# Kernel tuning notes

Hardware: AMD Instinct MI355X
Metric: run time of the kernel (lower is better)

## Reference

```python
import jax, jax.numpy as jnp
import numpy as np
import math

GRID = 14  # coords run 1..13 -> 13x13 spatial grid
Z = math.exp(math.log(2.0 * math.pi) + 1.0)
EPS = 1e-06

def setup_inputs() -> dict:
    key = jax.random.key(0)
    B, C = 256, 1024
    x = jax.random.normal(key, (B, GRID - 1, GRID - 1, C), dtype=jnp.float32)
    return {"feature_input": x}

def reference(feature_input) -> jnp.ndarray:
    B, H, W, C = feature_input.shape
    f = jax.nn.softmax(feature_input, axis=3)  # softmax over channel dim (dim=3)
    coords = jnp.arange(1, GRID, dtype=jnp.float32)  # [13]
    xv = coords[:, None]  # varies along spatial axis 0 (torch meshgrid 'ij')
    yv = coords[None, :]  # varies along spatial axis 1
    s = f.sum(axis=(1, 2)) + EPS  # [B, C] per-slice mass
    # soft-argmax centroids, [B, C]
    mx = (xv[None, :, :, None] * f).sum(axis=(1, 2)) / s
    my = (yv[None, :, :, None] * f).sum(axis=(1, 2)) / s
    # weighted variances, normalized by 169 and the per-slice mass
    dx2 = (xv[None, :, :, None] - mx[:, None, None, :]) ** 2
    dy2 = (yv[None, :, :, None] - my[:, None, None, :]) ** 2
    x_var = (dx2 * f).sum(axis=(1, 2)) / 169.0 / s
    y_var = (dy2 * f).sum(axis=(1, 2)) / 169.0 / s
    det_xy = (x_var + y_var) ** 2 * Z  # [B, C]
    return det_xy.sum() / B / C
```

## Files before the change

kernel.cpp:

```cpp
#include <hip/hip_runtime.h>

#ifndef __has_builtin
#define __has_builtin(x) 0
#endif

__device__ __forceinline__ float fast_exp2(float x) {
#if __has_builtin(__builtin_amdgcn_exp2f)
    return __builtin_amdgcn_exp2f(x);
#else
    return exp2f(x);
#endif
}

__device__ __forceinline__ float fast_log2(float x) {
#if __has_builtin(__builtin_amdgcn_logf)
    return __builtin_amdgcn_logf(x);
#else
    return log2f(x);
#endif
}

constexpr int   kB      = 256;
constexpr int   kC      = 1024;
constexpr int   kG      = 13;
constexpr int   kP      = kG * kG;
constexpr float kEps    = 1e-6f;
constexpr float kZ      = 17.079468445347132f;
constexpr float kLog2e  = 1.4426950408889634f;
constexpr float kInv169 = 1.0f / 169.0f;
constexpr float kScale  = 1.0f / (256.0f * 1024.0f);

__global__ __launch_bounds__(1024, 4)
void constrain_loss_fused(const float* __restrict__ x, float* __restrict__ out)
{
    __shared__ float snL[kP];
    __shared__ float sred[16];

    const int tid  = threadIdx.x;
    const int lane = tid & 63;
    const int wid  = tid >> 6;
    const int b    = blockIdx.x;

    const float* __restrict__ xb = x + (size_t)b * kP * kC;

    for (int p = wid; p < kP; p += 16) {
        const float4* __restrict__ src = (const float4*)(xb + (size_t)p * kC);
        float4 v0 = src[lane];
        float4 v1 = src[lane + 64];
        float4 v2 = src[lane + 128];
        float4 v3 = src[lane + 192];

        float s =
            (fast_exp2(v0.x * kLog2e) + fast_exp2(v0.y * kLog2e)) +
            (fast_exp2(v0.z * kLog2e) + fast_exp2(v0.w * kLog2e)) +
            (fast_exp2(v1.x * kLog2e) + fast_exp2(v1.y * kLog2e)) +
            (fast_exp2(v1.z * kLog2e) + fast_exp2(v1.w * kLog2e)) +
            (fast_exp2(v2.x * kLog2e) + fast_exp2(v2.y * kLog2e)) +
            (fast_exp2(v2.z * kLog2e) + fast_exp2(v2.w * kLog2e)) +
            (fast_exp2(v3.x * kLog2e) + fast_exp2(v3.y * kLog2e)) +
            (fast_exp2(v3.z * kLog2e) + fast_exp2(v3.w * kLog2e));

        #pragma unroll
        for (int m = 1; m < 64; m <<= 1)
            s += __shfl_xor(s, m);

        if (lane == 0) snL[p] = -fast_log2(s);
    }
    __syncthreads();

    const float* __restrict__ xc = xb + tid;

    float S0 = 0.f, S1x = 0.f, S2x = 0.f, S1y = 0.f, S2y = 0.f;

    #pragma unroll
    for (int h = 0; h < kG; ++h) {
        const float* __restrict__ row = xc + (size_t)h * kG * kC;
        float v[kG];
        #pragma unroll
        for (int w = 0; w < kG; ++w)
            v[w] = row[(size_t)w * kC];

        float t0 = 0.f, t1 = 0.f, t2 = 0.f;
        #pragma unroll
        for (int w = 0; w < kG; ++w) {
            const float e = fast_exp2(fmaf(v[w], kLog2e, snL[h * kG + w]));
            t0 += e;
            t1 = fmaf((float)(w + 1), e, t1);
            t2 = fmaf((float)((w + 1) * (w + 1)), e, t2);
        }
        const float fx = (float)(h + 1);
        S0  += t0;
        S1x  = fmaf(fx,      t0, S1x);
        S2x  = fmaf(fx * fx, t0, S2x);
        S1y += t1;
        S2y += t2;
    }

    const float s   = S0 + kEps;
    const float is  = 1.0f / s;
    const float mx  = S1x * is;
    const float my  = S1y * is;
    const float nx  = S2x - mx * (2.0f * S1x - mx * S0);
    const float ny  = S2y - my * (2.0f * S1y - my * S0);
    const float t   = (nx + ny) * is * kInv169;
    float det = t * t * kZ;

    #pragma unroll
    for (int m = 1; m < 64; m <<= 1)
        det += __shfl_xor(det, m);

    if (lane == 0) sred[wid] = det;
    __syncthreads();
    if (wid == 0) {
        float v = (lane < 16) ? sred[lane] : 0.0f;
        #pragma unroll
        for (int m = 1; m < 16; m <<= 1)
            v += __shfl_xor(v, m);
        if (lane == 0) atomicAdd(out, v * kScale);
    }
}

extern "C" void kernel_launch(void* const* d_in, const int* in_sizes, int n_in,
                              void* d_out, int out_size, void* d_ws, size_t ws_size,
                              hipStream_t stream)
{
    const float* x   = (const float*)d_in[0];
    float*       out = (float*)d_out;

    hipMemsetAsync(out, 0, sizeof(float) * (size_t)out_size, stream);
    constrain_loss_fused<<<dim3(kB), dim3(1024), 0, stream>>>(x, out);
}
```

Measured before the change: 263.7 us.

## Split spatial positions across four blocks per batch with register-resident single pass

Each batch is split into four blocks over spatial positions. Each thread keeps its exp values in registers, so the input is read and exponentiated once instead of twice. Partial moments go to a workspace and a second kernel combines them into the loss. This raises block count for better occupancy, at the cost of an extra launch, workspace traffic and possible register pressure.

```diff
diff --git a/kernel.cpp b/kernel.cpp
--- a/kernel.cpp
+++ b/kernel.cpp
@@ -12,18 +12,12 @@
 #endif
 }
 
-__device__ __forceinline__ float fast_log2(float x) {
-#if __has_builtin(__builtin_amdgcn_logf)
-    return __builtin_amdgcn_logf(x);
-#else
-    return log2f(x);
-#endif
-}
-
 constexpr int   kB      = 256;
 constexpr int   kC      = 1024;
 constexpr int   kG      = 13;
 constexpr int   kP      = kG * kG;
+constexpr int   kParts  = 4;
+constexpr int   kMaxPP  = 43;
 constexpr float kEps    = 1e-6f;
 constexpr float kZ      = 17.079468445347132f;
 constexpr float kLog2e  = 1.4426950408889634f;
@@ -31,9 +25,83 @@
 constexpr float kScale  = 1.0f / (256.0f * 1024.0f);
 
 __global__ __launch_bounds__(1024, 4)
-void constrain_loss_fused(const float* __restrict__ x, float* __restrict__ out)
+void part_stats_kernel(const float* __restrict__ x, float* __restrict__ ws)
 {
-    __shared__ float snL[kP];
+    __shared__ float4 sTab[kP];
+    __shared__ float  sP[kMaxPP * 16];
+    __shared__ float  sInvD[kMaxPP];
+
+    const int tid   = threadIdx.x;
+    const int lane  = tid & 63;
+    const int wid   = tid >> 6;
+    const int b     = blockIdx.x >> 2;
+    const int part  = blockIdx.x & 3;
+    const int start = part * 42;
+    const bool full = (part == 3);
+
+    if (tid < kP) {
+        const int h = tid / kG;
+        const int w = tid - h * kG;
+        const float fx = (float)(h + 1);
+        const float fy = (float)(w + 1);
+        sTab[tid] = make_float4(fx, fy, fx * fx, fy * fy);
+    }
+
+    const float* __restrict__ xc = x + (size_t)b * kP * kC + (size_t)start * kC + tid;
+
+    float e[kMaxPP];
+    #pragma unroll
+    for (int i = 0; i < kMaxPP; ++i)
+        e[i] = xc[(size_t)i * kC];
+
+    #pragma unroll
+    for (int i = 0; i < kMaxPP; ++i)
+        e[i] = fast_exp2(e[i] * kLog2e);
+
+    if (!full) e[42] = 0.0f;
+
+    #pragma unroll
+    for (int i = 0; i < kMaxPP; ++i) {
+        float s = e[i];
+        #pragma unroll
+        for (int m = 1; m < 64; m <<= 1)
+            s += __shfl_xor(s, m);
+        if (lane == 0) sP[i * 16 + wid] = s;
+    }
+    __syncthreads();
+
+    if (tid < kMaxPP) {
+        float d = 0.f;
+        #pragma unroll
+        for (int w = 0; w < 16; ++w)
+            d += sP[tid * 16 + w];
+        sInvD[tid] = 1.0f / (d + 1e-30f);
+    }
+    __syncthreads();
+
+    float S0 = 0.f, S1x = 0.f, S1y = 0.f, S2x = 0.f, S2y = 0.f;
+    #pragma unroll
+    for (int i = 0; i < kMaxPP; ++i) {
+        const float  f = e[i] * sInvD[i];
+        const float4 t = sTab[start + i];
+        S0  += f;
+        S1x  = fmaf(t.x, f, S1x);
+        S1y  = fmaf(t.y, f, S1y);
+        S2x  = fmaf(t.z, f, S2x);
+        S2y  = fmaf(t.w, f, S2y);
+    }
+
+    float* __restrict__ o = ws + (((size_t)part * kB + b) * 5) * kC + tid;
+    o[0 * kC] = S0;
+    o[1 * kC] = S1x;
+    o[2 * kC] = S1y;
+    o[3 * kC] = S2x;
+    o[4 * kC] = S2y;
+}
+
+__global__ __launch_bounds__(1024, 4)
+void combine_kernel(const float* __restrict__ ws, float* __restrict__ out)
+{
     __shared__ float sred[16];
 
     const int tid  = threadIdx.x;
@@ -41,59 +109,15 @@
     const int wid  = tid >> 6;
     const int b    = blockIdx.x;
 
-    const float* __restrict__ xb = x + (size_t)b * kP * kC;
-
-    for (int p = wid; p < kP; p += 16) {
-        const float4* __restrict__ src = (const float4*)(xb + (size_t)p * kC);
-        float4 v0 = src[lane];
-        float4 v1 = src[lane + 64];
-        float4 v2 = src[lane + 128];
-        float4 v3 = src[lane + 192];
-
-        float s =
-            (fast_exp2(v0.x * kLog2e) + fast_exp2(v0.y * kLog2e)) +
-            (fast_exp2(v0.z * kLog2e) + fast_exp2(v0.w * kLog2e)) +
-            (fast_exp2(v1.x * kLog2e) + fast_exp2(v1.y * kLog2e)) +
-            (fast_exp2(v1.z * kLog2e) + fast_exp2(v1.w * kLog2e)) +
-            (fast_exp2(v2.x * kLog2e) + fast_exp2(v2.y * kLog2e)) +
-            (fast_exp2(v2.z * kLog2e) + fast_exp2(v2.w * kLog2e)) +
-            (fast_exp2(v3.x * kLog2e) + fast_exp2(v3.y * kLog2e)) +
-            (fast_exp2(v3.z * kLog2e) + fast_exp2(v3.w * kLog2e));
-
-        #pragma unroll
-        for (int m = 1; m < 64; m <<= 1)
-            s += __shfl_xor(s, m);
-
-        if (lane == 0) snL[p] = -fast_log2(s);
-    }
-    __syncthreads();
-
-    const float* __restrict__ xc = xb + tid;
-
-    float S0 = 0.f, S1x = 0.f, S2x = 0.f, S1y = 0.f, S2y = 0.f;
-
+    float S0 = 0.f, S1x = 0.f, S1y = 0.f, S2x = 0.f, S2y = 0.f;
     #pragma unroll
-    for (int h = 0; h < kG; ++h) {
-        const float* __restrict__ row = xc + (size_t)h * kG * kC;
-        float v[kG];
-        #pragma unroll
-        for (int w = 0; w < kG; ++w)
-            v[w] = row[(size_t)w * kC];
-
-        float t0 = 0.f, t1 = 0.f, t2 = 0.f;
-        #pragma unroll
-        for (int w = 0; w < kG; ++w) {
-            const float e = fast_exp2(fmaf(v[w], kLog2e, snL[h * kG + w]));
-            t0 += e;
-            t1 = fmaf((float)(w + 1), e, t1);
-            t2 = fmaf((float)((w + 1) * (w + 1)), e, t2);
-        }
-        const float fx = (float)(h + 1);
-        S0  += t0;
-        S1x  = fmaf(fx,      t0, S1x);
-        S2x  = fmaf(fx * fx, t0, S2x);
-        S1y += t1;
-        S2y += t2;
+    for (int part = 0; part < kParts; ++part) {
+        const float* __restrict__ o = ws + (((size_t)part * kB + b) * 5) * kC + tid;
+        S0  += o[0 * kC];
+        S1x += o[1 * kC];
+        S1y += o[2 * kC];
+        S2x += o[3 * kC];
+        S2y += o[4 * kC];
     }
 
     const float s   = S0 + kEps;
@@ -126,7 +150,9 @@
 {
     const float* x   = (const float*)d_in[0];
     float*       out = (float*)d_out;
+    float*       ws  = (float*)d_ws;
 
     hipMemsetAsync(out, 0, sizeof(float) * (size_t)out_size, stream);
-    constrain_loss_fused<<<dim3(kB), dim3(1024), 0, stream>>>(x, out);
+    part_stats_kernel<<<dim3(kB * kParts), dim3(1024), 0, stream>>>(x, ws);
+    combine_kernel  <<<dim3(kB),           dim3(1024), 0, stream>>>(ws, out);
 }
```

Measured after the change: 276.2 us. 4.8% more time.

## Split into row-sum and moments kernels with finer grids and register prefetch

Applied to the files above, without the earlier changes.

Replaces the single per-batch fused kernel with a row-sum kernel that writes reciprocal softmax denominators to workspace and a moments kernel split into four channel chunks per batch. Both kernels use 256-thread blocks, giving many more blocks for better occupancy. The moments loop double-buffers the next spatial row's loads in registers. The change trades an extra full pass over the input through global memory (plus a workspace round trip) for higher parallelism and latency hiding.

```diff
diff --git a/kernel.cpp b/kernel.cpp
--- a/kernel.cpp
+++ b/kernel.cpp
@@ -12,78 +12,86 @@
 #endif
 }
 
-__device__ __forceinline__ float fast_log2(float x) {
-#if __has_builtin(__builtin_amdgcn_logf)
-    return __builtin_amdgcn_logf(x);
-#else
-    return log2f(x);
-#endif
-}
-
 constexpr int   kB      = 256;
 constexpr int   kC      = 1024;
 constexpr int   kG      = 13;
 constexpr int   kP      = kG * kG;
+constexpr int   kRows   = kB * kP;
 constexpr float kEps    = 1e-6f;
 constexpr float kZ      = 17.079468445347132f;
 constexpr float kLog2e  = 1.4426950408889634f;
 constexpr float kInv169 = 1.0f / 169.0f;
 constexpr float kScale  = 1.0f / (256.0f * 1024.0f);
 
-__global__ __launch_bounds__(1024, 4)
-void constrain_loss_fused(const float* __restrict__ x, float* __restrict__ out)
+__global__ __launch_bounds__(256, 8)
+void rowsum_kernel(const float* __restrict__ x, float* __restrict__ invD)
 {
-    __shared__ float snL[kP];
-    __shared__ float sred[16];
-
     const int tid  = threadIdx.x;
     const int lane = tid & 63;
     const int wid  = tid >> 6;
-    const int b    = blockIdx.x;
+    const int row  = blockIdx.x * 4 + wid;
 
-    const float* __restrict__ xb = x + (size_t)b * kP * kC;
+    const float4* __restrict__ src = (const float4*)(x + (size_t)row * kC);
+    float4 v0 = src[lane];
+    float4 v1 = src[lane + 64];
+    float4 v2 = src[lane + 128];
+    float4 v3 = src[lane + 192];
 
-    for (int p = wid; p < kP; p += 16) {
-        const float4* __restrict__ src = (const float4*)(xb + (size_t)p * kC);
-        float4 v0 = src[lane];
-        float4 v1 = src[lane + 64];
-        float4 v2 = src[lane + 128];
-        float4 v3 = src[lane + 192];
+    float s =
+        (fast_exp2(v0.x * kLog2e) + fast_exp2(v0.y * kLog2e)) +
+        (fast_exp2(v0.z * kLog2e) + fast_exp2(v0.w * kLog2e)) +
+        (fast_exp2(v1.x * kLog2e) + fast_exp2(v1.y * kLog2e)) +
+        (fast_exp2(v1.z * kLog2e) + fast_exp2(v1.w * kLog2e)) +
+        (fast_exp2(v2.x * kLog2e) + fast_exp2(v2.y * kLog2e)) +
+        (fast_exp2(v2.z * kLog2e) + fast_exp2(v2.w * kLog2e)) +
+        (fast_exp2(v3.x * kLog2e) + fast_exp2(v3.y * kLog2e)) +
+        (fast_exp2(v3.z * kLog2e) + fast_exp2(v3.w * kLog2e));
 
-        float s =
-            (fast_exp2(v0.x * kLog2e) + fast_exp2(v0.y * kLog2e)) +
-            (fast_exp2(v0.z * kLog2e) + fast_exp2(v0.w * kLog2e)) +
-            (fast_exp2(v1.x * kLog2e) + fast_exp2(v1.y * kLog2e)) +
-            (fast_exp2(v1.z * kLog2e) + fast_exp2(v1.w * kLog2e)) +
-            (fast_exp2(v2.x * kLog2e) + fast_exp2(v2.y * kLog2e)) +
-            (fast_exp2(v2.z * kLog2e) + fast_exp2(v2.w * kLog2e)) +
-            (fast_exp2(v3.x * kLog2e) + fast_exp2(v3.y * kLog2e)) +
-            (fast_exp2(v3.z * kLog2e) + fast_exp2(v3.w * kLog2e));
+    #pragma unroll
+    for (int m = 1; m < 64; m <<= 1)
+        s += __shfl_xor(s, m);
 
-        #pragma unroll
-        for (int m = 1; m < 64; m <<= 1)
-            s += __shfl_xor(s, m);
+    if (lane == 0) invD[row] = 1.0f / s;
+}
 
-        if (lane == 0) snL[p] = -fast_log2(s);
-    }
+__global__ __launch_bounds__(256, 8)
+void moments_kernel(const float* __restrict__ x, const float* __restrict__ invD,
+                    float* __restrict__ out)
+{
+    __shared__ float sInv[kP];
+    __shared__ float sred[4];
+
+    const int tid   = threadIdx.x;
+    const int lane  = tid & 63;
+    const int wid   = tid >> 6;
+    const int b     = blockIdx.x >> 2;
+    const int chunk = blockIdx.x & 3;
+
+    if (tid < kP) sInv[tid] = invD[b * kP + tid];
     __syncthreads();
 
-    const float* __restrict__ xc = xb + tid;
+    const float* __restrict__ xc = x + (size_t)b * kP * kC + chunk * 256 + tid;
 
     float S0 = 0.f, S1x = 0.f, S2x = 0.f, S1y = 0.f, S2y = 0.f;
 
+    float v[kG], vn[kG];
     #pragma unroll
+    for (int w = 0; w < kG; ++w)
+        v[w] = xc[(size_t)w * kC];
+
+    #pragma unroll 1
     for (int h = 0; h < kG; ++h) {
-        const float* __restrict__ row = xc + (size_t)h * kG * kC;
-        float v[kG];
-        #pragma unroll
-        for (int w = 0; w < kG; ++w)
-            v[w] = row[(size_t)w * kC];
+        if (h + 1 < kG) {
+            const float* __restrict__ rn = xc + (size_t)(h + 1) * kG * kC;
+            #pragma unroll
+            for (int w = 0; w < kG; ++w)
+                vn[w] = rn[(size_t)w * kC];
+        }
 
         float t0 = 0.f, t1 = 0.f, t2 = 0.f;
         #pragma unroll
         for (int w = 0; w < kG; ++w) {
-            const float e = fast_exp2(fmaf(v[w], kLog2e, snL[h * kG + w]));
+            const float e = fast_exp2(v[w] * kLog2e) * sInv[h * kG + w];
             t0 += e;
             t1 = fmaf((float)(w + 1), e, t1);
             t2 = fmaf((float)((w + 1) * (w + 1)), e, t2);
@@ -94,6 +102,10 @@
         S2x  = fmaf(fx * fx, t0, S2x);
         S1y += t1;
         S2y += t2;
+
+        #pragma unroll
+        for (int w = 0; w < kG; ++w)
+            v[w] = vn[w];
     }
 
     const float s   = S0 + kEps;
@@ -111,22 +123,19 @@
 
     if (lane == 0) sred[wid] = det;
     __syncthreads();
-    if (wid == 0) {
-        float v = (lane < 16) ? sred[lane] : 0.0f;
-        #pragma unroll
-        for (int m = 1; m < 16; m <<= 1)
-            v += __shfl_xor(v, m);
-        if (lane == 0) atomicAdd(out, v * kScale);
-    }
+    if (tid == 0)
+        atomicAdd(out, (sred[0] + sred[1] + sred[2] + sred[3]) * kScale);
 }
 
 extern "C" void kernel_launch(void* const* d_in, const int* in_sizes, int n_in,
                               void* d_out, int out_size, void* d_ws, size_t ws_size,
                               hipStream_t stream)
 {
-    const float* x   = (const float*)d_in[0];
-    float*       out = (float*)d_out;
+    const float* x    = (const float*)d_in[0];
+    float*       out  = (float*)d_out;
+    float*       invD = (float*)d_ws;
 
     hipMemsetAsync(out, 0, sizeof(float) * (size_t)out_size, stream);
-    constrain_loss_fused<<<dim3(kB), dim3(1024), 0, stream>>>(x, out);
+    rowsum_kernel <<<dim3(kRows / 4), dim3(256), 0, stream>>>(x, invD);
+    moments_kernel<<<dim3(kB * 4),    dim3(256), 0, stream>>>(x, invD, out);
 }
```

After: 271.2 us. +2.9%, slower.
